# Performance work log

Measured on AMD Instinct MI355X. Metric: run time of the kernel, lower is better.

Reference implementation:

```python
import jax, jax.numpy as jnp
import numpy as np

H = 16            # num heads
D_NOPE = 128
D_ROPE = 64
D_V = 128
Q_LORA = 1536
KV_LORA = 512
HIDDEN = 2048
EPS = 1e-6


def rmsnorm(x, w):
    xf = x.astype(jnp.float32)
    var = jnp.mean(xf * xf, axis=-1, keepdims=True)
    return (w * (xf * jax.lax.rsqrt(var + EPS))).astype(x.dtype)


def rope_interleaved(x, cos, sin):
    # x: [B,H,S,D]; cos,sin: [S,D] -> use even-index entries as the per-pair values
    B, nH, S, D = x.shape
    cv = cos[:, 0::2].astype(jnp.float32)[None, None]  # [1,1,S,D/2]
    sv = sin[:, 0::2].astype(jnp.float32)[None, None]
    xf = x.astype(jnp.float32).reshape(B, nH, S, D // 2, 2)
    xr, xi = xf[..., 0], xf[..., 1]
    out = jnp.stack([xr * cv - xi * sv, xr * sv + xi * cv], axis=-1)
    return out.reshape(B, nH, S, D).astype(x.dtype)


def setup_inputs() -> dict:
    key = jax.random.key(0)
    ks = jax.random.split(key, 9)
    B, S = 2, 2048
    std = 0.02
    return {
        "hidden_states": jax.random.normal(ks[0], (B, S, HIDDEN), jnp.float32),
        "cos": jax.random.uniform(ks[1], (S, D_ROPE), jnp.float32),
        "sin": jax.random.uniform(ks[2], (S, D_ROPE), jnp.float32),
        "q_a_w": jax.random.normal(ks[3], (HIDDEN, Q_LORA), jnp.float32) * std,
        "q_a_ln_w": jnp.ones((Q_LORA,), jnp.float32),
        "q_b_w": jax.random.normal(ks[4], (Q_LORA, H * (D_NOPE + D_ROPE)), jnp.float32) * std,
        "kv_a_w": jax.random.normal(ks[5], (HIDDEN, KV_LORA + D_ROPE), jnp.float32) * std,
        "kv_a_ln_w": jnp.ones((KV_LORA,), jnp.float32),
        "kv_b_w": jax.random.normal(ks[6], (KV_LORA, H * (D_NOPE + D_V)), jnp.float32) * std,
        "o_w": jax.random.normal(ks[7], (H * D_V, HIDDEN), jnp.float32) * std,
    }


def reference(hidden_states, cos, sin, q_a_w, q_a_ln_w, q_b_w, kv_a_w, kv_a_ln_w, kv_b_w, o_w):
    B, S, _ = hidden_states.shape
    scale = 1.0 / np.sqrt(D_NOPE + D_ROPE)

    # Q path: low-rank down-proj, RMSNorm, up-proj
    q = rmsnorm(hidden_states @ q_a_w, q_a_ln_w) @ q_b_w
    q = q.reshape(B, S, H, D_NOPE + D_ROPE).transpose(0, 2, 1, 3)  # [B,H,S,Dq]
    q_nope, q_rope = q[..., :D_NOPE], q[..., D_NOPE:]

    # KV path: compressed kv + shared rope key
    ckv = hidden_states @ kv_a_w  # [B,S,KV_LORA+D_ROPE]
    compressed_kv, k_rope = ckv[..., :KV_LORA], ckv[..., KV_LORA:]
    k_rope = jnp.broadcast_to(k_rope[:, None], (B, H, S, D_ROPE))
    kv = rmsnorm(compressed_kv, kv_a_ln_w) @ kv_b_w
    kv = kv.reshape(B, S, H, D_NOPE + D_V).transpose(0, 2, 1, 3)  # [B,H,S,Dk+Dv]
    k_nope, value = kv[..., :D_NOPE], kv[..., D_NOPE:]

    q_rope = rope_interleaved(q_rope, cos, sin)
    k_rope = rope_interleaved(k_rope, cos, sin)

    query = jnp.concatenate([q_nope, q_rope], axis=-1)  # [B,H,S,192]
    key = jnp.concatenate([k_nope, k_rope], axis=-1)

    attn = jnp.einsum("bhqd,bhkd->bhqk", query, key) * scale
    attn = jax.nn.softmax(attn.astype(jnp.float32), axis=-1).astype(query.dtype)
    out = jnp.einsum("bhqk,bhkd->bhqd", attn, value)  # [B,H,S,Dv]
    out = out.transpose(0, 2, 1, 3).reshape(B, S, H * D_V)
    return out @ o_w
```

## Files before the change

kernel.cpp:

```cpp
#include <hip/hip_runtime.h>

typedef unsigned short u16;
typedef __bf16 bf16x8 __attribute__((ext_vector_type(8)));
typedef float f32x4 __attribute__((ext_vector_type(4)));
typedef u16 u16x4 __attribute__((ext_vector_type(4)));

#define S_ 2048

__device__ __forceinline__ u16 f2bf(float f) {
  union { float f; unsigned u; } v; v.f = f;
  unsigned r = v.u + 0x7fffu + ((v.u >> 16) & 1u);
  return (u16)(r >> 16);
}
__device__ __forceinline__ float bf2f(u16 h) {
  union { unsigned u; float f; } v; v.u = ((unsigned)h) << 16;
  return v.f;
}

__device__ __forceinline__ f32x4 mfma16(bf16x8 a, bf16x8 b, f32x4 c) {
  return __builtin_amdgcn_mfma_f32_16x16x32_bf16(a, b, c, 0, 0, 0);
}

__device__ __forceinline__ void async16(const void* g, void* l) {
  __builtin_amdgcn_global_load_lds((__attribute__((address_space(1))) void*)g,
                                   (__attribute__((address_space(3))) void*)l,
                                   16, 0, 0);
}

__global__ void cast_bf8_k(const float* __restrict__ in, u16* __restrict__ out, int n8) {
  int i = blockIdx.x * 256 + threadIdx.x;
  if (i < n8) {
    f32x4 a = ((const f32x4*)in)[2 * i], b = ((const f32x4*)in)[2 * i + 1];
    union { u16 v[8]; f32x4 q; } u;
#pragma unroll
    for (int e = 0; e < 4; ++e) { u.v[e] = f2bf(a[e]); u.v[4 + e] = f2bf(b[e]); }
    ((f32x4*)out)[i] = u.q;
  }
}

__global__ void transw_k(const float* __restrict__ W, u16* __restrict__ Wt,
                         int K, int N) {
  __shared__ float tile[32][33];
  int k0 = blockIdx.x * 32, n0 = blockIdx.y * 32;
  int tx = threadIdx.x, ty = threadIdx.y;
#pragma unroll
  for (int r = 0; r < 32; r += 8) {
    int n = n0 + tx;
    tile[ty + r][tx] = (n < N) ? W[(long)(k0 + ty + r) * N + n] : 0.f;
  }
  __syncthreads();
#pragma unroll
  for (int r = 0; r < 32; r += 8) {
    Wt[(long)(n0 + ty + r) * K + k0 + tx] = f2bf(tile[tx][ty + r]);
  }
}

__device__ __forceinline__ int xcd_chunk(int lin, int nwg) {
  if ((nwg & 7) == 0) return (lin & 7) * (nwg >> 3) + (lin >> 3);
  return lin;
}

template <typename OUT_T, bool ROPE>
__global__ __launch_bounds__(256)
void gemm_bt_k(const u16* __restrict__ A, const u16* __restrict__ Bt,
               OUT_T* __restrict__ C, int K, int Nc, int ldc,
               const float* __restrict__ cs, const float* __restrict__ sn) {
  __shared__ __align__(16) u16 sA[2][128 * 32];
  __shared__ __align__(16) u16 sB[2][128 * 32];
  int tid = threadIdx.x;
  int lane = tid & 63, w = tid >> 6;
  int wr = w >> 1, wc = w & 1;
  int l15 = lane & 15, quad = lane >> 4;
  int gx = gridDim.x;
  int nl = xcd_chunk(blockIdx.x + gx * blockIdx.y, gx * gridDim.y);
  long tm = (long)(nl / gx) * 128;
  long tn = (long)(nl % gx) * 128;
  const u16* Ab = A + tm * K;
  const u16* Bb = Bt + tn * K;
  f32x4 acc[4][4] = {};

#pragma unroll
  for (int it = 0; it < 2; ++it) {
    int c = tid + it * 256;
    int row = c >> 2, kc = c & 3;
    async16(Ab + (long)row * K + kc * 8, &sA[0][c * 8]);
    async16(Bb + (long)row * K + kc * 8, &sB[0][c * 8]);
  }

  int nk = K >> 5;
  for (int kt = 0; kt < nk; ++kt) {
    int cur = kt & 1;
    __syncthreads();
    if (kt + 1 < nk) {
      int k0n = (kt + 1) << 5;
#pragma unroll
      for (int it = 0; it < 2; ++it) {
        int c = tid + it * 256;
        int row = c >> 2, kc = c & 3;
        async16(Ab + (long)row * K + k0n + kc * 8, &sA[cur ^ 1][c * 8]);
        async16(Bb + (long)row * K + k0n + kc * 8, &sB[cur ^ 1][c * 8]);
      }
    }
    bf16x8 af[4], bfr[4];
#pragma unroll
    for (int i = 0; i < 4; ++i)
      af[i] = *(const bf16x8*)(&sA[cur][(wr * 64 + i * 16 + l15) * 32 + quad * 8]);
#pragma unroll
    for (int j = 0; j < 4; ++j)
      bfr[j] = *(const bf16x8*)(&sB[cur][(wc * 64 + j * 16 + l15) * 32 + quad * 8]);
#pragma unroll
    for (int i = 0; i < 4; ++i)
#pragma unroll
      for (int j = 0; j < 4; ++j)
        acc[i][j] = mfma16(af[i], bfr[j], acc[i][j]);
  }
#pragma unroll
  for (int i = 0; i < 4; ++i) {
#pragma unroll
    for (int j = 0; j < 4; ++j) {
      int col = (int)tn + wc * 64 + j * 16 + l15;
      if (col < Nc) {
        bool ropeT = false;
        int fi = 0;
        if constexpr (ROPE) {
          int d = col % 192;
          ropeT = (d >= 128);
          fi = (d - 128) & ~1;
        }
#pragma unroll
        for (int r = 0; r < 4; ++r) {
          long row = tm + wr * 64 + i * 16 + quad * 4 + r;
          float v = acc[i][j][r];
          if constexpr (ROPE) {
            float partner = __shfl_xor(v, 1);
            if (ropeT) {
              int si = (int)row & (S_ - 1);
              float cv = cs[si * 64 + fi], sv = sn[si * 64 + fi];
              v = (l15 & 1) ? (partner * sv + v * cv)
                            : (v * cv - partner * sv);
            }
          }
          if constexpr (sizeof(OUT_T) == 2) C[row * ldc + col] = f2bf(v);
          else                              C[row * ldc + col] = v;
        }
      }
    }
  }
}

__global__ __launch_bounds__(256)
void gemm_kvb_k(const u16* __restrict__ A, const u16* __restrict__ Bt,
                u16* __restrict__ kswz, u16* __restrict__ vswz) {
  const int K = 512;
  __shared__ __align__(16) u16 sA[2][128 * 32];
  __shared__ __align__(16) u16 sB[2][128 * 32];
  int tid = threadIdx.x;
  int lane = tid & 63, w = tid >> 6;
  int wr = w >> 1, wc = w & 1;
  int l15 = lane & 15, quad = lane >> 4;
  int gx = gridDim.x;
  int nl = xcd_chunk(blockIdx.x + gx * blockIdx.y, gx * gridDim.y);
  long tm = (long)(nl / gx) * 128;
  long tn = (long)(nl % gx) * 128;
  const u16* Ab = A + tm * K;
  const u16* Bb = Bt + tn * K;
  f32x4 acc[4][4] = {};

#pragma unroll
  for (int it = 0; it < 2; ++it) {
    int c = tid + it * 256;
    int row = c >> 2, kc = c & 3;
    async16(Ab + (long)row * K + kc * 8, &sA[0][c * 8]);
    async16(Bb + (long)row * K + kc * 8, &sB[0][c * 8]);
  }

  const int nk = K >> 5;
  for (int kt = 0; kt < nk; ++kt) {
    int cur = kt & 1;
    __syncthreads();
    if (kt + 1 < nk) {
      int k0n = (kt + 1) << 5;
#pragma unroll
      for (int it = 0; it < 2; ++it) {
        int c = tid + it * 256;
        int row = c >> 2, kc = c & 3;
        async16(Ab + (long)row * K + k0n + kc * 8, &sA[cur ^ 1][c * 8]);
        async16(Bb + (long)row * K + k0n + kc * 8, &sB[cur ^ 1][c * 8]);
      }
    }
    bf16x8 af[4], bfr[4];
#pragma unroll
    for (int i = 0; i < 4; ++i)
      af[i] = *(const bf16x8*)(&sA[cur][(wr * 64 + i * 16 + l15) * 32 + quad * 8]);
#pragma unroll
    for (int j = 0; j < 4; ++j)
      bfr[j] = *(const bf16x8*)(&sB[cur][(wc * 64 + j * 16 + l15) * 32 + quad * 8]);
#pragma unroll
    for (int i = 0; i < 4; ++i)
#pragma unroll
      for (int j = 0; j < 4; ++j)
        acc[i][j] = mfma16(af[i], bfr[j], acc[i][j]);
  }

  int h = (int)(tn >> 8);
  int b = (int)(tm >> 11);
  int tile = (b * 16 + h) * 32 + (((int)tm & 2047) >> 6) + wr;
  if ((tn & 255) == 0) {
    u16* dst = kswz + (long)tile * 12288;
#pragma unroll
    for (int i = 0; i < 4; ++i) {
#pragma unroll
      for (int j = 0; j < 4; ++j) {
        int frag = quad * 6 + wc * 2 + (j >> 1);
        int chunk = frag * 64 + ((j & 1) * 2 + (l15 >> 3)) * 16 + i * 4;
#pragma unroll
        for (int r = 0; r < 4; ++r)
          dst[(chunk + r) * 8 + (l15 & 7)] = f2bf(acc[i][j][r]);
      }
    }
  } else {
    u16* dst = vswz + (long)tile * 8192;
    int kq = quad >> 1;
    int e0 = (quad & 1) * 4;
#pragma unroll
    for (int i = 0; i < 4; ++i) {
#pragma unroll
      for (int j = 0; j < 4; ++j) {
        int frag = kq * 8 + wc * 4 + j;
        u16x4 pk;
#pragma unroll
        for (int r = 0; r < 4; ++r) pk[r] = f2bf(acc[i][j][r]);
        *(u16x4*)(dst + (frag * 64 + i * 16 + l15) * 8 + e0) = pk;
      }
    }
  }
}

__global__ __launch_bounds__(256)
void rmsnorm2_k(const float* __restrict__ qsrc, int ldq,
                const float* __restrict__ kvsrc, int ldkv,
                const float* __restrict__ wq, const float* __restrict__ wkv,
                u16* __restrict__ qout, u16* __restrict__ kvout) {
  int blk = blockIdx.x;
  const float* x; const float* wt; u16* o; int N;
  if (blk < 4096) { x = qsrc + (long)blk * ldq;  wt = wq;  o = qout + (long)blk * 1536;  N = 1536; }
  else { blk -= 4096; x = kvsrc + (long)blk * ldkv; wt = wkv; o = kvout + (long)blk * 512; N = 512; }
  float ss = 0.f;
  for (int i = threadIdx.x; i < N; i += 256) { float v = x[i]; ss += v * v; }
#pragma unroll
  for (int off = 32; off; off >>= 1) ss += __shfl_down(ss, off);
  __shared__ float red[4];
  if ((threadIdx.x & 63) == 0) red[threadIdx.x >> 6] = ss;
  __syncthreads();
  float inv = rsqrtf((red[0] + red[1] + red[2] + red[3]) / N + 1e-6f);
  for (int i = threadIdx.x; i < N; i += 256) o[i] = f2bf(wt[i] * x[i] * inv);
}

__global__ void krope_k(const float* __restrict__ src, int ld,
                        const float* __restrict__ cs, const float* __restrict__ sn,
                        u16* __restrict__ out) {
  int idx = blockIdx.x * 256 + threadIdx.x;
  int row = idx >> 5, i = idx & 31;
  int s = row & (S_ - 1);
  float xr = src[(long)row * ld + 2 * i];
  float xi = src[(long)row * ld + 2 * i + 1];
  float cv = cs[s * 64 + 2 * i], sv = sn[s * 64 + 2 * i];
  out[(long)row * 64 + 2 * i]     = f2bf(xr * cv - xi * sv);
  out[(long)row * 64 + 2 * i + 1] = f2bf(xr * sv + xi * cv);
}

__global__ void krfill_k(const u16* __restrict__ kr, u16* __restrict__ kswz) {
  int tile = blockIdx.x;
  int bh = tile >> 5, kt = tile & 31;
  int b = bh >> 4;
  u16* dst = kswz + (long)tile * 12288;
#pragma unroll
  for (int it = 0; it < 2; ++it) {
    int c = threadIdx.x + it * 256;
    int lane = c & 63, fd = c >> 6;
    int kg = fd >> 1, dbr = fd & 1;
    int sl = lane & 15;
    int key = kt * 64 + (sl >> 2) * 16 + kg * 4 + (sl & 3);
    int doff = dbr * 32 + (lane >> 4) * 8;
    int frag = kg * 6 + 4 + dbr;
    *(f32x4*)(dst + (frag * 64 + lane) * 8) =
        *(const f32x4*)(kr + ((long)(b * S_ + key)) * 64 + doff);
  }
}

__global__ __launch_bounds__(256, 2)
void attn_k(const u16* __restrict__ qb, const u16* __restrict__ kswz,
            const u16* __restrict__ vswz, u16* __restrict__ attnO) {
  int lin = blockIdx.x + 16 * blockIdx.y;
  int xcd = lin & 7;
  int j = lin >> 3;
  int bh = (xcd << 2) + (j >> 4);
  int qt = j & 15;
  int b = bh >> 4, h = bh & 15;
  int tid = threadIdx.x, lane = tid & 63, w = tid >> 6;
  int l15 = lane & 15, quad = lane >> 4;
  int qrow0 = qt * 128 + w * 32;

  __shared__ __align__(16) u16 sK[2][24 * 64 * 8];
  __shared__ __align__(16) u16 sV[2][16 * 64 * 8];

  const u16* Kb = kswz + (long)bh * 32 * 12288;
  const u16* Vb = vswz + (long)bh * 32 * 8192;

  bf16x8 qf[2][6];
#pragma unroll
  for (int rg = 0; rg < 2; ++rg) {
    const u16* qp = qb + ((long)(b * S_ + qrow0 + rg * 16 + l15)) * 3072 + h * 192 + quad * 8;
#pragma unroll
    for (int kb = 0; kb < 6; ++kb) qf[rg][kb] = *(const bf16x8*)(qp + kb * 32);
  }

  f32x4 o[2][8] = {};
  float lsum[2] = {};
  const float scale = 0.07216878364870322f;

#pragma unroll
  for (int i = 0; i < 6; ++i) { int c = tid + i * 256; async16(Kb + c * 8, &sK[0][c * 8]); }
#pragma unroll
  for (int i = 0; i < 4; ++i) { int c = tid + i * 256; async16(Vb + c * 8, &sV[0][c * 8]); }

#pragma unroll 1
  for (int kt = 0; kt < 32; ++kt) {
    int cur = kt & 1;
    __syncthreads();
    if (kt < 31) {
      const u16* Kt = Kb + (long)(kt + 1) * 12288;
      const u16* Vt = Vb + (long)(kt + 1) * 8192;
#pragma unroll
      for (int i = 0; i < 6; ++i) { int c = tid + i * 256; async16(Kt + c * 8, &sK[cur ^ 1][c * 8]); }
#pragma unroll
      for (int i = 0; i < 4; ++i) { int c = tid + i * 256; async16(Vt + c * 8, &sV[cur ^ 1][c * 8]); }
    }

    const u16* kbase = sK[cur];
    const u16* vbase = sV[cur];

    f32x4 s[2][4] = {};
#pragma unroll
    for (int kg = 0; kg < 4; ++kg) {
#pragma unroll
      for (int db = 0; db < 6; ++db) {
        bf16x8 kf = *(const bf16x8*)(kbase + ((kg * 6 + db) * 64 + lane) * 8);
        s[0][kg] = mfma16(kf, qf[0][db], s[0][kg]);
        s[1][kg] = mfma16(kf, qf[1][db], s[1][kg]);
      }
    }

    bf16x8 pf[2][2];
#pragma unroll
    for (int rg = 0; rg < 2; ++rg) {
#pragma unroll
      for (int kg = 0; kg < 4; ++kg) {
#pragma unroll
        for (int r = 0; r < 4; ++r) {
          float p = __expf(s[rg][kg][r] * scale);
          lsum[rg] += p;
          s[rg][kg][r] = p;
        }
      }
#pragma unroll
      for (int kq = 0; kq < 2; ++kq) {
        union { unsigned wd[4]; bf16x8 v; } u;
        asm("v_cvt_pk_bf16_f32 %0, %1, %2"
            : "=v"(u.wd[0]) : "v"(s[rg][2 * kq][0]), "v"(s[rg][2 * kq][1]));
        asm("v_cvt_pk_bf16_f32 %0, %1, %2"
            : "=v"(u.wd[1]) : "v"(s[rg][2 * kq][2]), "v"(s[rg][2 * kq][3]));
        asm("v_cvt_pk_bf16_f32 %0, %1, %2"
            : "=v"(u.wd[2]) : "v"(s[rg][2 * kq + 1][0]), "v"(s[rg][2 * kq + 1][1]));
        asm("v_cvt_pk_bf16_f32 %0, %1, %2"
            : "=v"(u.wd[3]) : "v"(s[rg][2 * kq + 1][2]), "v"(s[rg][2 * kq + 1][3]));
        pf[rg][kq] = u.v;
      }
    }

#pragma unroll
    for (int kq = 0; kq < 2; ++kq) {
#pragma unroll
      for (int j2 = 0; j2 < 8; ++j2) {
        bf16x8 vf = *(const bf16x8*)(vbase + ((kq * 8 + j2) * 64 + lane) * 8);
        o[0][j2] = mfma16(pf[0][kq], vf, o[0][j2]);
        o[1][j2] = mfma16(pf[1][kq], vf, o[1][j2]);
      }
    }
  }

  float invr[2][4];
#pragma unroll
  for (int rg = 0; rg < 2; ++rg) {
    float ssum = lsum[rg];
    ssum += __shfl_xor(ssum, 16);
    ssum += __shfl_xor(ssum, 32);
#pragma unroll
    for (int r = 0; r < 4; ++r)
      invr[rg][r] = 1.f / __shfl(ssum, quad * 4 + r);
  }
#pragma unroll
  for (int rg = 0; rg < 2; ++rg) {
    u16* op = attnO + ((long)(b * S_ + qrow0 + rg * 16)) * 2048 + h * 128;
#pragma unroll
    for (int j2 = 0; j2 < 8; ++j2)
#pragma unroll
      for (int r = 0; r < 4; ++r)
        op[(long)(quad * 4 + r) * 2048 + j2 * 16 + l15] = f2bf(o[rg][j2][r] * invr[rg][r]);
  }
}

extern "C" void kernel_launch(void* const* d_in, const int* in_sizes, int n_in,
                              void* d_out, int out_size, void* d_ws, size_t ws_size,
                              hipStream_t stream) {
  const float* hs      = (const float*)d_in[0];
  const float* cosb    = (const float*)d_in[1];
  const float* sinb    = (const float*)d_in[2];
  const float* q_a_w   = (const float*)d_in[3];
  const float* q_a_ln  = (const float*)d_in[4];
  const float* q_b_w   = (const float*)d_in[5];
  const float* kv_a_w  = (const float*)d_in[6];
  const float* kv_a_ln = (const float*)d_in[7];
  const float* kv_b_w  = (const float*)d_in[8];
  const float* o_w     = (const float*)d_in[9];
  float* out = (float*)d_out;
  (void)in_sizes; (void)n_in; (void)out_size; (void)ws_size;

  char* p = (char*)d_ws;
  auto alloc = [&](size_t b) { char* r = p; p += (b + 255) & ~((size_t)255); return r; };
  u16*   hs_bf  = (u16*)  alloc((size_t)4096 * 2048 * 2);
  u16*   qakvT  = (u16*)  alloc((size_t)2176 * 2048 * 2);
  u16*   qbwT   = (u16*)  alloc((size_t)3072 * 1536 * 2);
  u16*   kvbwT  = (u16*)  alloc((size_t)4096 * 512  * 2);
  u16*   owT    = (u16*)  alloc((size_t)2048 * 2048 * 2);
  float* qa_ckv = (float*)alloc((size_t)4096 * 2176 * 4);
  u16*   qan    = (u16*)  alloc((size_t)4096 * 1536 * 2);
  u16*   ckvn   = (u16*)  alloc((size_t)4096 * 512  * 2);
  u16*   kr     = (u16*)  alloc((size_t)4096 * 64   * 2);
  u16*   qbuf   = (u16*)  alloc((size_t)4096 * 3072 * 2);
  u16*   aO     = (u16*)  alloc((size_t)4096 * 2048 * 2);
  u16* kswz = (u16*)qa_ckv;
  u16* vswz = (u16*)hs_bf;

  dim3 tb(32, 8);
  cast_bf8_k<<<4096, 256, 0, stream>>>(hs, hs_bf, 4096 * 2048 / 8);
  transw_k<<<dim3(64, 48),  tb, 0, stream>>>(q_a_w,  qakvT,                     2048, 1536);
  transw_k<<<dim3(64, 20),  tb, 0, stream>>>(kv_a_w, qakvT + (long)1536 * 2048, 2048, 576);
  transw_k<<<dim3(48, 96),  tb, 0, stream>>>(q_b_w,  qbwT,  1536, 3072);
  transw_k<<<dim3(16, 128), tb, 0, stream>>>(kv_b_w, kvbwT, 512,  4096);
  transw_k<<<dim3(64, 64),  tb, 0, stream>>>(o_w,    owT,   2048, 2048);

  gemm_bt_k<float, false><<<dim3(17, 32), 256, 0, stream>>>(
      hs_bf, qakvT, qa_ckv, 2048, 2176, 2176, nullptr, nullptr);
  rmsnorm2_k<<<8192, 256, 0, stream>>>(qa_ckv, 2176, qa_ckv + 1536, 2176,
                                       q_a_ln, kv_a_ln, qan, ckvn);
  krope_k<<<512, 256, 0, stream>>>(qa_ckv + 2048, 2176, cosb, sinb, kr);
  gemm_bt_k<u16, true><<<dim3(24, 32), 256, 0, stream>>>(
      qan, qbwT, qbuf, 1536, 3072, 3072, cosb, sinb);
  gemm_kvb_k<<<dim3(32, 32), 256, 0, stream>>>(ckvn, kvbwT, kswz, vswz);
  krfill_k<<<1024, 256, 0, stream>>>(kr, kswz);
  attn_k<<<dim3(16, 32), 256, 0, stream>>>(qbuf, kswz, vswz, aO);
  gemm_bt_k<float, false><<<dim3(16, 32), 256, 0, stream>>>(
      aO, owT, out, 2048, 2048, 2048, nullptr, nullptr);
}
```

Measured before the change: 473.2 us.

## Enlarge GEMM tiles to 256x256 with K-step 64 and XOR-swizzled LDS

Replaces the 128x128, 256-thread bf16 GEMM with a 256x256, 512-thread version that stages 64-wide K slices into an XOR-swizzled shared buffer. Each wave now accumulates an 8x4 grid of MFMA tiles. The aim is more operand reuse per LDS load, fewer global loads per FLOP, and fewer LDS bank conflicts. The q_a/kv_a weight buffer is padded to 2304 rows so 256-wide N tiles stay in bounds. The cost is that the three GEMMs now launch only 128–192 blocks, fewer than the CU count, and each block uses about 128 KB of LDS, so occupancy and machine fill drop.

```diff
diff --git a/kernel.cpp b/kernel.cpp
--- a/kernel.cpp
+++ b/kernel.cpp
@@ -61,61 +61,67 @@
 }
 
 template <typename OUT_T, bool ROPE>
-__global__ __launch_bounds__(256)
-void gemm_bt_k(const u16* __restrict__ A, const u16* __restrict__ Bt,
-               OUT_T* __restrict__ C, int K, int Nc, int ldc,
-               const float* __restrict__ cs, const float* __restrict__ sn) {
-  __shared__ __align__(16) u16 sA[2][128 * 32];
-  __shared__ __align__(16) u16 sB[2][128 * 32];
+__global__ __launch_bounds__(512, 2)
+void gemm256_bt_k(const u16* __restrict__ A, const u16* __restrict__ Bt,
+                  OUT_T* __restrict__ C, int K, int Nc, int ldc,
+                  const float* __restrict__ cs, const float* __restrict__ sn) {
+  __shared__ __align__(16) u16 sA[2][256 * 64];
+  __shared__ __align__(16) u16 sB[2][256 * 64];
   int tid = threadIdx.x;
   int lane = tid & 63, w = tid >> 6;
-  int wr = w >> 1, wc = w & 1;
+  int wr = w >> 2, wc = w & 3;
   int l15 = lane & 15, quad = lane >> 4;
   int gx = gridDim.x;
   int nl = xcd_chunk(blockIdx.x + gx * blockIdx.y, gx * gridDim.y);
-  long tm = (long)(nl / gx) * 128;
-  long tn = (long)(nl % gx) * 128;
+  long tm = (long)(nl / gx) * 256;
+  long tn = (long)(nl % gx) * 256;
   const u16* Ab = A + tm * K;
   const u16* Bb = Bt + tn * K;
-  f32x4 acc[4][4] = {};
-
-#pragma unroll
-  for (int it = 0; it < 2; ++it) {
-    int c = tid + it * 256;
-    int row = c >> 2, kc = c & 3;
-    async16(Ab + (long)row * K + kc * 8, &sA[0][c * 8]);
-    async16(Bb + (long)row * K + kc * 8, &sB[0][c * 8]);
-  }
-
-  int nk = K >> 5;
+  f32x4 acc[8][4] = {};
+
+#define STAGE256(buf, kk)                                                   \
+  {                                                                         \
+    int k0_ = (kk) << 6;                                                    \
+    _Pragma("unroll")                                                       \
+    for (int it = 0; it < 4; ++it) {                                        \
+      int c = tid + it * 512;                                               \
+      int row = c >> 3, sl = c & 7;                                         \
+      int kc = k0_ + ((sl ^ (row & 7)) << 3);                               \
+      async16(Ab + (long)row * K + kc, &sA[buf][c * 8]);                    \
+      async16(Bb + (long)row * K + kc, &sB[buf][c * 8]);                    \
+    }                                                                       \
+  }
+
+  STAGE256(0, 0);
+  int nk = K >> 6;
   for (int kt = 0; kt < nk; ++kt) {
     int cur = kt & 1;
     __syncthreads();
-    if (kt + 1 < nk) {
-      int k0n = (kt + 1) << 5;
-#pragma unroll
-      for (int it = 0; it < 2; ++it) {
-        int c = tid + it * 256;
-        int row = c >> 2, kc = c & 3;
-        async16(Ab + (long)row * K + k0n + kc * 8, &sA[cur ^ 1][c * 8]);
-        async16(Bb + (long)row * K + k0n + kc * 8, &sB[cur ^ 1][c * 8]);
-      }
-    }
-    bf16x8 af[4], bfr[4];
-#pragma unroll
-    for (int i = 0; i < 4; ++i)
-      af[i] = *(const bf16x8*)(&sA[cur][(wr * 64 + i * 16 + l15) * 32 + quad * 8]);
-#pragma unroll
-    for (int j = 0; j < 4; ++j)
-      bfr[j] = *(const bf16x8*)(&sB[cur][(wc * 64 + j * 16 + l15) * 32 + quad * 8]);
-#pragma unroll
-    for (int i = 0; i < 4; ++i)
-#pragma unroll
-      for (int j = 0; j < 4; ++j)
-        acc[i][j] = mfma16(af[i], bfr[j], acc[i][j]);
-  }
-#pragma unroll
-  for (int i = 0; i < 4; ++i) {
+    if (kt + 1 < nk) STAGE256(cur ^ 1, kt + 1);
+#pragma unroll
+    for (int ks = 0; ks < 2; ++ks) {
+      bf16x8 bfr[4];
+#pragma unroll
+      for (int j = 0; j < 4; ++j) {
+        int rowb = wc * 64 + j * 16 + l15;
+        int slot = (ks * 4 + quad) ^ (rowb & 7);
+        bfr[j] = *(const bf16x8*)(&sB[cur][rowb * 64 + slot * 8]);
+      }
+#pragma unroll
+      for (int i = 0; i < 8; ++i) {
+        int rowa = wr * 128 + i * 16 + l15;
+        int slot = (ks * 4 + quad) ^ (rowa & 7);
+        bf16x8 af = *(const bf16x8*)(&sA[cur][rowa * 64 + slot * 8]);
+#pragma unroll
+        for (int j = 0; j < 4; ++j)
+          acc[i][j] = mfma16(af, bfr[j], acc[i][j]);
+      }
+    }
+  }
+#undef STAGE256
+
+#pragma unroll
+  for (int i = 0; i < 8; ++i) {
 #pragma unroll
     for (int j = 0; j < 4; ++j) {
       int col = (int)tn + wc * 64 + j * 16 + l15;
@@ -129,7 +135,7 @@
         }
 #pragma unroll
         for (int r = 0; r < 4; ++r) {
-          long row = tm + wr * 64 + i * 16 + quad * 4 + r;
+          long row = tm + wr * 128 + i * 16 + quad * 4 + r;
           float v = acc[i][j][r];
           if constexpr (ROPE) {
             float partner = __shfl_xor(v, 1);
@@ -429,7 +435,7 @@
   char* p = (char*)d_ws;
   auto alloc = [&](size_t b) { char* r = p; p += (b + 255) & ~((size_t)255); return r; };
   u16*   hs_bf  = (u16*)  alloc((size_t)4096 * 2048 * 2);
-  u16*   qakvT  = (u16*)  alloc((size_t)2176 * 2048 * 2);
+  u16*   qakvT  = (u16*)  alloc((size_t)2304 * 2048 * 2);
   u16*   qbwT   = (u16*)  alloc((size_t)3072 * 1536 * 2);
   u16*   kvbwT  = (u16*)  alloc((size_t)4096 * 512  * 2);
   u16*   owT    = (u16*)  alloc((size_t)2048 * 2048 * 2);
@@ -450,16 +456,16 @@
   transw_k<<<dim3(16, 128), tb, 0, stream>>>(kv_b_w, kvbwT, 512,  4096);
   transw_k<<<dim3(64, 64),  tb, 0, stream>>>(o_w,    owT,   2048, 2048);
 
-  gemm_bt_k<float, false><<<dim3(17, 32), 256, 0, stream>>>(
+  gemm256_bt_k<float, false><<<dim3(9, 16), 512, 0, stream>>>(
       hs_bf, qakvT, qa_ckv, 2048, 2176, 2176, nullptr, nullptr);
   rmsnorm2_k<<<8192, 256, 0, stream>>>(qa_ckv, 2176, qa_ckv + 1536, 2176,
                                        q_a_ln, kv_a_ln, qan, ckvn);
   krope_k<<<512, 256, 0, stream>>>(qa_ckv + 2048, 2176, cosb, sinb, kr);
-  gemm_bt_k<u16, true><<<dim3(24, 32), 256, 0, stream>>>(
+  gemm256_bt_k<u16, true><<<dim3(12, 16), 512, 0, stream>>>(
       qan, qbwT, qbuf, 1536, 3072, 3072, cosb, sinb);
   gemm_kvb_k<<<dim3(32, 32), 256, 0, stream>>>(ckvn, kvbwT, kswz, vswz);
   krfill_k<<<1024, 256, 0, stream>>>(kr, kswz);
   attn_k<<<dim3(16, 32), 256, 0, stream>>>(qbuf, kswz, vswz, aO);
-  gemm_bt_k<float, false><<<dim3(16, 32), 256, 0, stream>>>(
+  gemm256_bt_k<float, false><<<dim3(8, 16), 512, 0, stream>>>(
       aO, owT, out, 2048, 2048, 2048, nullptr, nullptr);
 }
```

New measurement: 529.3 us. +11.8%, slower.
